# Performance work log

Measured on AMD Instinct MI355X. Metric: run time of the kernel, lower is better.

Reference implementation:

```python
import jax, jax.numpy as jnp
import numpy as np

B, N, IN_C, HID, K1, K2, OUT_C = 128, 512, 128, 32, 100, 10, 10
E_PER = 8192  # edges per graph (avg degree 16)
EPS = 1e-15


def _lin(key, fan_in, fan_out):
    return jax.random.normal(key, (fan_in, fan_out), jnp.float32) / np.sqrt(fan_in)


def setup_inputs() -> dict:
    key = jax.random.key(0)
    ks = jax.random.split(key, 20)
    total = B * N
    x = jax.random.normal(ks[0], (total, IN_C), jnp.float32)
    # per-graph random edges, offset into the global node index space
    src_l = jax.random.randint(ks[1], (B, E_PER), 0, N)
    dst_l = jax.random.randint(ks[2], (B, E_PER), 0, N)
    off = (jnp.arange(B, dtype=jnp.int32) * N)[:, None]
    edge_index = jnp.stack([(src_l + off).reshape(-1), (dst_l + off).reshape(-1)]).astype(jnp.int32)
    batch = (jnp.arange(total, dtype=jnp.int32) // N).astype(jnp.int32)
    return {
        "x": x,
        "edge_index": edge_index,
        "batch": batch,
        "conv1_W": _lin(ks[3], IN_C, HID), "conv1_b": jnp.zeros((HID,), jnp.float32),
        "pool1_W": _lin(ks[4], HID, K1), "pool1_b": jnp.zeros((K1,), jnp.float32),
        "conv2_rel_W": _lin(ks[5], HID, HID), "conv2_rel_b": jnp.zeros((HID,), jnp.float32),
        "conv2_root_W": _lin(ks[6], HID, HID),
        "pool2_W": _lin(ks[7], HID, K2), "pool2_b": jnp.zeros((K2,), jnp.float32),
        "conv3_rel_W": _lin(ks[8], HID, HID), "conv3_rel_b": jnp.zeros((HID,), jnp.float32),
        "conv3_root_W": _lin(ks[9], HID, HID),
        "lin1_W": _lin(ks[10], HID, HID), "lin1_b": jnp.zeros((HID,), jnp.float32),
        "lin2_W": _lin(ks[11], HID, OUT_C), "lin2_b": jnp.zeros((OUT_C,), jnp.float32),
    }


def gcn_conv(x, edge_index, W, b):
    # GCNConv with add_self_loops=True, symmetric normalization
    total = x.shape[0]
    loops = jnp.arange(total, dtype=edge_index.dtype)
    src = jnp.concatenate([edge_index[0], loops])
    dst = jnp.concatenate([edge_index[1], loops])
    w = jnp.ones(src.shape[0], x.dtype)
    deg = jax.ops.segment_sum(w, dst, num_segments=total)
    dis = jnp.where(deg > 0, jax.lax.rsqrt(deg), 0.0)
    norm = dis[src] * dis[dst]
    xw = x @ W
    out = jax.ops.segment_sum(norm[:, None] * xw[src], dst, num_segments=total)
    return out + b


def dense_mincut_pool(x, adj, s, mask=None):
    # x:[b,n,f] adj:[b,n,n] s:[b,n,k]
    s = jax.nn.softmax(s, axis=-1)
    if mask is not None:
        m = mask[..., None].astype(x.dtype)
        x = x * m
        s = s * m
    out = jnp.einsum('bnk,bnf->bkf', s, x)
    out_adj = jnp.einsum('bnk,bnm,bml->bkl', s, adj, s)
    mincut_num = jnp.trace(out_adj, axis1=-2, axis2=-1)
    d_flat = adj.sum(-1)  # [b,n]
    mincut_den = jnp.einsum('bnk,bn,bnk->b', s, d_flat, s)  # trace(s^T D s)
    mincut_loss = jnp.mean(-(mincut_num / mincut_den))
    k = s.shape[-1]
    ss = jnp.einsum('bnk,bnl->bkl', s, s)
    ss_norm = jnp.linalg.norm(ss, axis=(-1, -2), keepdims=True)
    i_s = jnp.eye(k, dtype=x.dtype) / jnp.sqrt(jnp.asarray(k, x.dtype))  # I_k / ||I_k||_F
    ortho_loss = jnp.mean(jnp.linalg.norm(ss / ss_norm - i_s, axis=(-1, -2)))
    # zero diagonal then symmetric degree-normalize
    out_adj = out_adj * (1.0 - jnp.eye(k, dtype=x.dtype))
    d = jnp.sqrt(out_adj.sum(-1))[..., None] + EPS
    out_adj = out_adj / d / jnp.swapaxes(d, -1, -2)
    return out, out_adj, mincut_loss, ortho_loss


def dense_graph_conv(x, adj, rel_W, rel_b, root_W):
    # DenseGraphConv(aggr='add'): lin_rel(adj @ x) + lin_root(x)
    return (adj @ x) @ rel_W + rel_b + x @ root_W


def reference(x, edge_index, batch, conv1_W, conv1_b, pool1_W, pool1_b,
              conv2_rel_W, conv2_rel_b, conv2_root_W, pool2_W, pool2_b,
              conv3_rel_W, conv3_rel_b, conv3_root_W, lin1_W, lin1_b, lin2_W, lin2_b):
    h = jax.nn.relu(gcn_conv(x, edge_index, conv1_W, conv1_b))
    # to_dense_batch: sorted batch with N nodes per graph -> reshape; mask all-true
    xd = h.reshape(B, N, HID)
    mask = jnp.ones((B, N), bool)
    # to_dense_adj
    b_idx = edge_index[0] // N
    s_l = edge_index[0] % N
    d_l = edge_index[1] % N
    adj = jnp.zeros((B, N, N), x.dtype).at[b_idx, s_l, d_l].add(1.0)
    s = xd @ pool1_W + pool1_b
    xd, adj, mc1, o1 = dense_mincut_pool(xd, adj, s, mask)
    xd = jax.nn.relu(dense_graph_conv(xd, adj, conv2_rel_W, conv2_rel_b, conv2_root_W))
    s = xd @ pool2_W + pool2_b
    xd, adj, mc2, o2 = dense_mincut_pool(xd, adj, s)
    xd = dense_graph_conv(xd, adj, conv3_rel_W, conv3_rel_b, conv3_root_W)
    g = xd.mean(axis=1)  # [B, HID]
    g = jax.nn.relu(g @ lin1_W + lin1_b)
    g = g @ lin2_W + lin2_b
    return jax.nn.log_softmax(g, axis=-1), mc1 + mc2 + o1 + o2
```

## Files before the change

### kernel.cpp

```cpp
#include <hip/hip_runtime.h>
#include <hip/hip_bf16.h>

#define TB   128
#define NN   512
#define INC  128
#define HH   32
#define KP1  100
#define KP2  10
#define OC   10
#define EPER 8192
#define NT   (TB*NN)
#define ET   (TB*EPER)
#define ZTR  264
#define ZTS  40
#define XTS  136

typedef unsigned int  u32;
typedef unsigned short u16;
typedef __attribute__((ext_vector_type(8))) short bf16x8;
typedef __attribute__((ext_vector_type(16))) float f32x16;

__device__ __forceinline__ u32 bfr(float f) {
    u32 b = __float_as_uint(f);
    return (b + 0x7fffu + ((b >> 16) & 1u)) >> 16;
}
__device__ __forceinline__ u32 pk2(float a, float b) { return bfr(a) | (bfr(b) << 16); }
__device__ __forceinline__ float blo(u32 u) { return __uint_as_float(u << 16); }
__device__ __forceinline__ float bhi(u32 u) { return __uint_as_float(u & 0xffff0000u); }

__global__ void k_init(float* __restrict__ aux) {
    int i = blockIdx.x * 256 + threadIdx.x;
    if (i < 1024) aux[i] = 0.0f;
}

__global__ __launch_bounds__(1024) void k_sort(const int* __restrict__ ei,
                                               int* __restrict__ cnt_src, int* __restrict__ cnt_dst,
                                               int* __restrict__ off_src, int* __restrict__ off_dst,
                                               u16* __restrict__ srt_dst, u16* __restrict__ srt_src,
                                               float* __restrict__ dis) {
    __shared__ int hs[NN], hd[NN], ps[NN], pd[NN];
    __shared__ __align__(16) u16 sdl[EPER], ssl[EPER];
    int g = blockIdx.x, tid = threadIdx.x, goff = g * NN;
    if (tid < NN) { hs[tid] = 0; hd[tid] = 0; }
    __syncthreads();
    const int* es = ei + (size_t)g * EPER;
    const int* ed = ei + ET + (size_t)g * EPER;
    for (int e = tid; e < EPER; e += 1024) {
        atomicAdd(&hs[es[e] - goff], 1);
        atomicAdd(&hd[ed[e] - goff], 1);
    }
    __syncthreads();
    int vs = 0, vd = 0;
    if (tid < NN) { vs = hs[tid]; vd = hd[tid]; ps[tid] = vs; pd[tid] = vd; }
    __syncthreads();
    for (int off = 1; off < NN; off <<= 1) {
        int xa = 0, xb = 0;
        if (tid < NN) {
            xa = ps[tid]; xb = pd[tid];
            if (tid >= off) { xa += ps[tid - off]; xb += pd[tid - off]; }
        }
        __syncthreads();
        if (tid < NN) { ps[tid] = xa; pd[tid] = xb; }
        __syncthreads();
    }
    int eso = 0, edo = 0;
    if (tid < NN) {
        eso = ps[tid] - vs; edo = pd[tid] - vd;
        cnt_src[goff + tid] = vs;  cnt_dst[goff + tid] = vd;
        off_src[goff + tid] = g * EPER + eso;
        off_dst[goff + tid] = g * EPER + edo;
        dis[goff + tid] = rsqrtf(1.0f + (float)vd);
    }
    __syncthreads();
    if (tid < NN) { ps[tid] = eso; pd[tid] = edo; }
    __syncthreads();
    for (int e = tid; e < EPER; e += 1024) {
        int s = es[e] - goff, d = ed[e] - goff;
        int p = atomicAdd(&ps[s], 1); sdl[p] = (u16)d;
        int q = atomicAdd(&pd[d], 1); ssl[q] = (u16)s;
    }
    __syncthreads();
    u32* wd = (u32*)(srt_dst + (size_t)g * EPER);
    u32* ws = (u32*)(srt_src + (size_t)g * EPER);
    const u32* rd = (const u32*)sdl;
    const u32* rs = (const u32*)ssl;
    for (int i = tid; i < EPER / 2; i += 1024) { wd[i] = rd[i]; ws[i] = rs[i]; }
}

__global__ __launch_bounds__(256) void k_xw2(const float* __restrict__ x, const float* __restrict__ W,
                                             u16* __restrict__ xwb) {
    __shared__ u16 sX[128 * XTS];
    __shared__ u16 sW[32 * XTS];
    int tid = threadIdx.x;
    int nbase = blockIdx.x * 128;
    for (int i = tid; i < INC * HH; i += 256) {
        int k = i >> 5, n = i & 31;
        sW[n * XTS + k] = (u16)bfr(W[i]);
    }
    for (int i = tid; i < 128 * 32; i += 256) {
        int r = i >> 5, q = i & 31;
        float4 v = ((const float4*)(x + (size_t)(nbase + r) * INC))[q];
        u32* dst = (u32*)&sX[r * XTS + q * 4];
        dst[0] = pk2(v.x, v.y);
        dst[1] = pk2(v.z, v.w);
    }
    __syncthreads();
    int wave = tid >> 6, lane = tid & 63;
    int lc = lane & 31, half = lane >> 5;
    f32x16 acc;
#pragma unroll
    for (int r = 0; r < 16; r++) acc[r] = 0.f;
#pragma unroll
    for (int kc = 0; kc < 8; kc++) {
        bf16x8 af  = *(const bf16x8*)&sX[(wave * 32 + lc) * XTS + kc * 16 + half * 8];
        bf16x8 bfv = *(const bf16x8*)&sW[lc * XTS + kc * 16 + half * 8];
        acc = __builtin_amdgcn_mfma_f32_32x32x16_bf16(af, bfv, acc, 0, 0, 0);
    }
#pragma unroll
    for (int r = 0; r < 16; r++) {
        int m = (r & 3) + 8 * (r >> 2) + 4 * half;
        int rowg = nbase + wave * 32 + m;
        xwb[(size_t)rowg * HH + lc] = (u16)bfr(acc[r]);
    }
}

__global__ __launch_bounds__(256) void k_gcng(const u16* __restrict__ ssrc, const int* __restrict__ od,
                                              const int* __restrict__ cd, const u32* __restrict__ xwb32,
                                              const float* __restrict__ dis, const float* __restrict__ bias,
                                              u32* __restrict__ hb32) {
    int tid = threadIdx.x;
    int b = blockIdx.x;
    int r8 = b & 7, j = b >> 3;
    int g = r8 + 8 * (j & 15);
    int chunk = j >> 4;
    int n = g * NN + chunk * 16 + (tid >> 4), cp = tid & 15;
    int goff = g * NN;
    int base = od[n], cnt = cd[n];
    float dn = dis[n];
    u32 us = xwb32[(size_t)n * 16 + cp];
    float a0 = dn * blo(us), a1 = dn * bhi(us);
    int i = 0;
    for (; i + 4 <= cnt; i += 4) {
        int s0 = goff + ssrc[base + i],     s1v = goff + ssrc[base + i + 1];
        int s2 = goff + ssrc[base + i + 2], s3  = goff + ssrc[base + i + 3];
        float d0 = dis[s0], d1 = dis[s1v], d2 = dis[s2], d3 = dis[s3];
        u32 u0 = xwb32[(size_t)s0 * 16 + cp];
        u32 u1 = xwb32[(size_t)s1v * 16 + cp];
        u32 u2 = xwb32[(size_t)s2 * 16 + cp];
        u32 u3 = xwb32[(size_t)s3 * 16 + cp];
        a0 += d0 * blo(u0) + d1 * blo(u1) + d2 * blo(u2) + d3 * blo(u3);
        a1 += d0 * bhi(u0) + d1 * bhi(u1) + d2 * bhi(u2) + d3 * bhi(u3);
    }
    for (; i < cnt; i++) {
        int s0 = goff + ssrc[base + i]; float d0 = dis[s0];
        u32 u0 = xwb32[(size_t)s0 * 16 + cp];
        a0 += d0 * blo(u0); a1 += d0 * bhi(u0);
    }
    float v0 = fmaxf(dn * a0 + bias[2 * cp], 0.f);
    float v1 = fmaxf(dn * a1 + bias[2 * cp + 1], 0.f);
    hb32[(size_t)n * 16 + cp] = pk2(v0, v1);
}

__global__ __launch_bounds__(256) void k_s1m(const u32* __restrict__ hb32, const float* __restrict__ W,
                                             const float* __restrict__ bias, const int* __restrict__ csrc,
                                             u16* __restrict__ s1b, float* __restrict__ den1) {
    __shared__ u16 sH[128 * ZTS];
    __shared__ u16 sW[128 * ZTS];
    int tid = threadIdx.x;
    int nbase = blockIdx.x * 128;
    for (int i = tid; i < HH * KP1; i += 256) {
        int k = i / KP1, n = i - k * KP1;
        sW[n * ZTS + k] = (u16)bfr(W[i]);
    }
    for (int i = tid; i < 28 * 16; i += 256) {
        int n = 100 + (i >> 4), q = i & 15;
        ((u32*)sW)[n * (ZTS / 2) + q] = 0;
    }
    for (int i = tid; i < 128 * 16; i += 256) {
        int r = i >> 4, q = i & 15;
        ((u32*)sH)[r * (ZTS / 2) + q] = hb32[(size_t)(nbase + r) * 16 + q];
    }
    __syncthreads();
    int wave = tid >> 6, lane = tid & 63;
    int lc = lane & 31, half = lane >> 5;
    f32x16 acc[4];
#pragma unroll
    for (int t = 0; t < 4; t++)
#pragma unroll
        for (int r = 0; r < 16; r++) acc[t][r] = 0.f;
#pragma unroll
    for (int kc = 0; kc < 2; kc++) {
        bf16x8 af = *(const bf16x8*)&sH[(wave * 32 + lc) * ZTS + kc * 16 + half * 8];
#pragma unroll
        for (int t = 0; t < 4; t++) {
            bf16x8 bfv = *(const bf16x8*)&sW[(t * 32 + lc) * ZTS + kc * 16 + half * 8];
            acc[t] = __builtin_amdgcn_mfma_f32_32x32x16_bf16(af, bfv, acc[t], 0, 0, 0);
        }
    }
    float s[16], q[16];
#pragma unroll
    for (int r = 0; r < 16; r++) { s[r] = 0.f; q[r] = 0.f; }
#pragma unroll
    for (int t = 0; t < 4; t++) {
        int ch = t * 32 + lc;
        bool valid = ch < KP1;
        float bv = valid ? bias[ch] : 0.f;
#pragma unroll
        for (int r = 0; r < 16; r++) {
            float ev = valid ? __expf(acc[t][r] + bv) : 0.f;
            acc[t][r] = ev; s[r] += ev; q[r] = fmaf(ev, ev, q[r]);
        }
    }
#pragma unroll
    for (int off = 16; off >= 1; off >>= 1) {
#pragma unroll
        for (int r = 0; r < 16; r++) { s[r] += __shfl_xor(s[r], off); q[r] += __shfl_xor(q[r], off); }
    }
    float inv[16];
#pragma unroll
    for (int r = 0; r < 16; r++) inv[r] = 1.f / s[r];
#pragma unroll
    for (int t = 0; t < 4; t++) {
        int ch = t * 32 + lc;
        if (ch < KP1) {
#pragma unroll
            for (int r = 0; r < 16; r++) {
                int lr = (r & 3) + 8 * (r >> 2) + 4 * half;
                int rowg = nbase + wave * 32 + lr;
                s1b[(size_t)rowg * KP1 + ch] = (u16)bfr(acc[t][r] * inv[r]);
            }
        }
    }
    float contrib = 0.f;
    if (lc == 0) {
#pragma unroll
        for (int r = 0; r < 16; r++) {
            int lr = (r & 3) + 8 * (r >> 2) + 4 * half;
            int rowg = nbase + wave * 32 + lr;
            contrib += (float)csrc[rowg] * q[r] * inv[r] * inv[r];
        }
    }
    contrib += __shfl_xor(contrib, 32);
    if (lane == 0) atomicAdd(&den1[nbase >> 9], contrib);
}

__global__ __launch_bounds__(256) void k_t1g(const u16* __restrict__ sdst, const int* __restrict__ osr,
                                             const int* __restrict__ csr, const u32* __restrict__ s1b32,
                                             u32* __restrict__ t1b32) {
    int tid = threadIdx.x;
    int b = blockIdx.x;
    int r8 = b & 7, j = b >> 3;
    int g = r8 + 8 * (j & 15);
    int chunk = j >> 4;
    int n = g * NN + chunk * 4 + (tid >> 6), lane = tid & 63;
    if (lane >= 50) return;
    int goff = g * NN;
    int base = osr[n], cnt = csr[n];
    float a0 = 0.f, a1 = 0.f;
    int i = 0;
    for (; i + 4 <= cnt; i += 4) {
        int d0 = goff + sdst[base + i],     d1 = goff + sdst[base + i + 1];
        int d2 = goff + sdst[base + i + 2], d3 = goff + sdst[base + i + 3];
        u32 u0 = s1b32[(size_t)d0 * 50 + lane];
        u32 u1 = s1b32[(size_t)d1 * 50 + lane];
        u32 u2 = s1b32[(size_t)d2 * 50 + lane];
        u32 u3 = s1b32[(size_t)d3 * 50 + lane];
        a0 += (blo(u0) + blo(u1)) + (blo(u2) + blo(u3));
        a1 += (bhi(u0) + bhi(u1)) + (bhi(u2) + bhi(u3));
    }
    for (; i < cnt; i++) {
        int d0 = goff + sdst[base + i];
        u32 u0 = s1b32[(size_t)d0 * 50 + lane];
        a0 += blo(u0); a1 += bhi(u0);
    }
    t1b32[(size_t)n * 50 + lane] = pk2(a0, a1);
}

__device__ __forceinline__ void ld_cp(const u32* __restrict__ sp, int rstr,
                                      u32& w0, u32& w1, u32& w2, u32& w3) {
    w0 = sp[0]; w1 = sp[rstr]; w2 = sp[2 * rstr]; w3 = sp[3 * rstr];
}
__device__ __forceinline__ void st_cp(u16* __restrict__ zb, int doff,
                                      u32 w0, u32 w1, u32 w2, u32 w3) {
    u32 lo01 = (w0 & 0xffffu) | (w1 << 16);
    u32 lo23 = (w2 & 0xffffu) | (w3 << 16);
    u32 hi01 = (w0 >> 16) | (w1 & 0xffff0000u);
    u32 hi23 = (w2 >> 16) | (w3 & 0xffff0000u);
    *(uint2*)&zb[doff]       = make_uint2(lo01, lo23);
    *(uint2*)&zb[doff + ZTS] = make_uint2(hi01, hi23);
}

#define GRAM_MFMA(zb)                                                                              \
    {                                                                                              \
        _Pragma("unroll")                                                                          \
        for (int mf = 0; mf < 2; mf++) {                                                           \
            bf16x8 af  = *(const bf16x8*)&(zb)[(132 + mt * 32 + lc) * ZTS + mf * 16 + half * 8];   \
            bf16x8 bv0 = *(const bf16x8*)&(zb)[((ct * 2    ) * 32 + lc) * ZTS + mf * 16 + half * 8]; \
            bf16x8 bv1 = *(const bf16x8*)&(zb)[((ct * 2 + 1) * 32 + lc) * ZTS + mf * 16 + half * 8]; \
            acc0 = __builtin_amdgcn_mfma_f32_32x32x16_bf16(af, bv0, acc0, 0, 0, 0);                \
            acc1 = __builtin_amdgcn_mfma_f32_32x32x16_bf16(af, bv1, acc1, 0, 0, 0);                \
        }                                                                                          \
    }

__global__ __launch_bounds__(1024, 1) void k_gram(const u32* __restrict__ s1b32, const u32* __restrict__ t1b32,
                                                  const u32* __restrict__ hb32,
                                                  float* __restrict__ A1n, float* __restrict__ P1,
                                                  float* __restrict__ aux) {
    __shared__ __align__(16) u16 sZ[2][ZTR * ZTS];
    __shared__ float sC[KP1 * 232];
    __shared__ float sRow[KP1], sd[KP1];
    __shared__ float sScal[3];
    int g = blockIdx.x;
    int nbase = g * NN;
    int tid = threadIdx.x;
    int wave = tid >> 6, lane = tid & 63;
    int mt = wave & 3;
    int ct = wave >> 2;
    int lc = lane & 31, half = lane >> 5;

    f32x16 acc0, acc1;
#pragma unroll
    for (int r = 0; r < 16; r++) { acc0[r] = 0.f; acc1[r] = 0.f; }

    int cp = (tid & 7) + ((tid >> 6) << 3);
    int rq = (tid >> 3) & 7;
    bool act = cp < 116;
    const u32* sp;
    int rstr;
    if (cp < 50)      { sp = t1b32 + cp;        rstr = 50; }
    else if (cp < 66) { sp = hb32 + (cp - 50);  rstr = 16; }
    else              { sp = s1b32 + (cp - 66); rstr = 50; }
    sp += (size_t)(nbase + rq * 4) * rstr;
    int step = rstr * 32;
    int doff = (2 * cp) * ZTS + rq * 4;

    if (tid < KP1) sRow[tid] = 0.f;
    if (tid < 3) sScal[tid] = 0.f;
    for (int i = tid; i < 32 * ZTS; i += 1024) {
        int r = 232 + i / ZTS, c = i % ZTS;
        sZ[0][r * ZTS + c] = 0; sZ[1][r * ZTS + c] = 0;
    }
    u32 a0, a1, a2, a3, b0 = 0, b1 = 0, b2 = 0, b3 = 0;
    if (act) {
        ld_cp(sp, rstr, a0, a1, a2, a3);
        st_cp(sZ[0], doff, a0, a1, a2, a3);
        sp += step;
        ld_cp(sp, rstr, b0, b1, b2, b3);
        sp += step;
    }
    __syncthreads();

    for (int nt = 0; nt < 16; nt += 2) {
        GRAM_MFMA(sZ[0]);
        if (act) {
            st_cp(sZ[1], doff, b0, b1, b2, b3);
            if (nt + 2 < 16) { ld_cp(sp, rstr, a0, a1, a2, a3); sp += step; }
        }
        __syncthreads();
        GRAM_MFMA(sZ[1]);
        if (act && nt + 2 < 16) {
            st_cp(sZ[0], doff, a0, a1, a2, a3);
            if (nt + 3 < 16) { ld_cp(sp, rstr, b0, b1, b2, b3); sp += step; }
        }
        __syncthreads();
    }
    {
        int l0 = (ct * 2) * 32 + lc;
        if (l0 < 232) {
#pragma unroll
            for (int r = 0; r < 16; r++) {
                int k = mt * 32 + (r & 3) + 8 * (r >> 2) + 4 * half;
                if (k < KP1) sC[k * 232 + l0] = acc0[r];
            }
        }
        int l1 = (ct * 2 + 1) * 32 + lc;
        if (l1 < 232) {
#pragma unroll
            for (int r = 0; r < 16; r++) {
                int k = mt * 32 + (r & 3) + 8 * (r >> 2) + 4 * half;
                if (k < KP1) sC[k * 232 + l1] = acc1[r];
            }
        }
    }
    __syncthreads();
    float ssq = 0.f, trss = 0.f, troa = 0.f;
    for (int idx = tid; idx < KP1 * 58; idx += 1024) {
        int k = idx / 58, q = idx - k * 58;
        float4 s = *(const float4*)&sC[k * 232 + q * 4];
        int c = q * 4;
        if (c < 100) {
            float rs = (s.x + s.y) + (s.z + s.w);
            if (k >= c && k < c + 4) { float d = ((const float*)&s)[k - c]; troa += d; rs -= d; }
            atomicAdd(&sRow[k], rs);
        } else if (c < 132) {
            *(float4*)&P1[((size_t)g * KP1 + k) * HH + (c - 100)] = s;
        } else {
            ssq += s.x * s.x + s.y * s.y + s.z * s.z + s.w * s.w;
            int l0 = c - 132;
            if (k >= l0 && k < l0 + 4) trss += ((const float*)&s)[k - l0];
        }
    }
#pragma unroll
    for (int off = 32; off >= 1; off >>= 1) {
        ssq  += __shfl_xor(ssq, off);
        trss += __shfl_xor(trss, off);
        troa += __shfl_xor(troa, off);
    }
    if ((tid & 63) == 0) {
        atomicAdd(&sScal[0], troa);
        atomicAdd(&sScal[1], trss);
        atomicAdd(&sScal[2], ssq);
    }
    __syncthreads();
    if (tid == 0) {
        float o1 = sqrtf(fmaxf(2.f - 2.f * sScal[1] / (sqrtf(sScal[2]) * 10.f), 0.f));
        aux[128 + g] = -(sScal[0] / aux[g]) + o1;
    }
    if (tid < KP1) sd[tid] = sqrtf(sRow[tid]) + 1e-15f;
    __syncthreads();
    for (int i = tid; i < KP1 * KP1; i += 1024) {
        int k = i / KP1, l = i - k * KP1;
        A1n[(size_t)g * (KP1 * KP1) + i] = (k == l) ? 0.f : sC[k * 232 + l] / (sd[k] * sd[l]);
    }
}

__global__ __launch_bounds__(512) void k_s2a(const float* __restrict__ A1n, const float* __restrict__ P1,
                                             const float* __restrict__ relW, const float* __restrict__ relB,
                                             const float* __restrict__ rootW,
                                             const float* __restrict__ p2W, const float* __restrict__ p2B,
                                             float* __restrict__ P2, float* __restrict__ A2n,
                                             float* __restrict__ aux) {
    __shared__ float sA[KP1 * KP1];
    __shared__ float sX[KP1 * HH];
    __shared__ float sY[KP1 * HH];
    __shared__ float sS2[KP1 * KP2];
    __shared__ float sT2[KP1 * KP2];
    __shared__ float sA2[100], sB2[100], sdd[10], red[100];
    int g = blockIdx.x, tid = threadIdx.x;
    const float* Ag = A1n + (size_t)g * (KP1 * KP1);
    for (int i = tid; i < KP1 * KP1 / 4; i += 512)
        ((float4*)sA)[i] = ((const float4*)Ag)[i];
    for (int i = tid; i < KP1 * HH; i += 512) sX[i] = P1[(size_t)g * (KP1 * HH) + i];
    __syncthreads();

    int n = tid >> 2, cq = tid & 3;
    if (tid < 400) {
        float yv[8];
#pragma unroll
        for (int j = 0; j < 8; j++) yv[j] = 0.f;
        for (int mq = 0; mq < 25; mq++) {
            float4 a4 = *(const float4*)&sA[n * KP1 + mq * 4];
            const float* xb = &sX[(mq * 4) * HH + cq * 8];
            float aa[4] = {a4.x, a4.y, a4.z, a4.w};
#pragma unroll
            for (int mm = 0; mm < 4; mm++) {
                const float* xr = xb + mm * HH;
#pragma unroll
                for (int j = 0; j < 8; j++) yv[j] = fmaf(aa[mm], xr[j], yv[j]);
            }
        }
#pragma unroll
        for (int j = 0; j < 8; j++) sY[n * HH + cq * 8 + j] = yv[j];
    }
    __syncthreads();
    float x2v[8];
    if (tid < 400) {
#pragma unroll
        for (int j = 0; j < 8; j++) x2v[j] = relB[cq * 8 + j];
        for (int j = 0; j < 32; j++) {
            float yj = sY[n * HH + j];
            float xj = sX[n * HH + j];
            float4 r0 = *(const float4*)&relW[j * 32 + cq * 8];
            float4 r1v = *(const float4*)&relW[j * 32 + cq * 8 + 4];
            float4 q0 = *(const float4*)&rootW[j * 32 + cq * 8];
            float4 q1 = *(const float4*)&rootW[j * 32 + cq * 8 + 4];
            x2v[0] += yj * r0.x + xj * q0.x;  x2v[1] += yj * r0.y + xj * q0.y;
            x2v[2] += yj * r0.z + xj * q0.z;  x2v[3] += yj * r0.w + xj * q0.w;
            x2v[4] += yj * r1v.x + xj * q1.x; x2v[5] += yj * r1v.y + xj * q1.y;
            x2v[6] += yj * r1v.z + xj * q1.z; x2v[7] += yj * r1v.w + xj * q1.w;
        }
    }
    __syncthreads();
    if (tid < 400) {
#pragma unroll
        for (int j = 0; j < 8; j++) sX[n * HH + cq * 8 + j] = fmaxf(x2v[j], 0.f);
    }
    __syncthreads();
    if (tid < KP1) {
        float lg[10];
#pragma unroll
        for (int j = 0; j < 10; j++) lg[j] = p2B[j];
        for (int c = 0; c < 32; c++) {
            float xv = sX[tid * HH + c];
#pragma unroll
            for (int j = 0; j < 10; j++) lg[j] = fmaf(xv, p2W[c * 10 + j], lg[j]);
        }
        float mx = lg[0];
#pragma unroll
        for (int j = 1; j < 10; j++) mx = fmaxf(mx, lg[j]);
        float se = 0.f;
#pragma unroll
        for (int j = 0; j < 10; j++) { lg[j] = __expf(lg[j] - mx); se += lg[j]; }
        float inv = 1.f / se, sq = 0.f;
#pragma unroll
        for (int j = 0; j < 10; j++) { float sv = lg[j] * inv; sS2[tid * 10 + j] = sv; sq += sv * sv; }
        float d2 = 0.f;
        for (int mq = 0; mq < 25; mq++) {
            float4 a4 = *(const float4*)&sA[tid * KP1 + mq * 4];
            d2 += a4.x + a4.y + a4.z + a4.w;
        }
        red[tid] = d2 * sq;
    }
    __syncthreads();
    for (int p = tid; p < KP1 * KP2; p += 512) {
        int n2 = p / 10, jj = p % 10;
        float a = 0.f;
        for (int m = 0; m < KP1; m++) a = fmaf(sA[n2 * KP1 + m], sS2[m * 10 + jj], a);
        sT2[p] = a;
    }
    if (tid < KP2 * HH) {
        int k = tid >> 5, cc = tid & 31;
        float a = 0.f;
        for (int n2 = 0; n2 < KP1; n2++) a = fmaf(sS2[n2 * 10 + k], sX[n2 * HH + cc], a);
        P2[(size_t)g * (KP2 * HH) + tid] = a;
    }
    __syncthreads();
    if (tid < 100) {
        int k = tid / 10, l = tid % 10;
        float oa = 0.f, ss = 0.f;
        for (int n2 = 0; n2 < KP1; n2++) {
            float sk = sS2[n2 * 10 + k];
            oa = fmaf(sk, sT2[n2 * 10 + l], oa);
            ss = fmaf(sk, sS2[n2 * 10 + l], ss);
        }
        sA2[tid] = oa; sB2[tid] = ss;
    }
    __syncthreads();
    if (tid == 0) {
        float den2 = 0.f;
        for (int i = 0; i < 100; i++) den2 += red[i];
        float troa = 0.f, trss = 0.f, ssq = 0.f;
        for (int k = 0; k < 10; k++) { troa += sA2[k * 10 + k]; trss += sB2[k * 10 + k]; }
        for (int i = 0; i < 100; i++) ssq += sB2[i] * sB2[i];
        float o2 = sqrtf(fmaxf(2.f - 2.f * trss / (sqrtf(ssq) * 3.16227766f), 0.f));
        aux[256 + g] = -(troa / den2) + o2;
    }
    if (tid < 10) {
        float rs = 0.f;
        for (int l = 0; l < 10; l++) if (l != tid) rs += sA2[tid * 10 + l];
        sdd[tid] = sqrtf(rs) + 1e-15f;
    }
    __syncthreads();
    if (tid < 100) {
        int k = tid / 10, l = tid % 10;
        A2n[(size_t)g * 100 + tid] = (k == l) ? 0.f : sA2[tid] / (sdd[k] * sdd[l]);
    }
}

__global__ __launch_bounds__(64) void k_s2b(const float* __restrict__ P2, const float* __restrict__ A2n,
                                            const float* __restrict__ relW3, const float* __restrict__ relb3,
                                            const float* __restrict__ rootW3,
                                            const float* __restrict__ l1W, const float* __restrict__ l1b,
                                            const float* __restrict__ l2W, const float* __restrict__ l2b,
                                            float* __restrict__ out) {
    __shared__ float sP[KP2 * HH], sA2[100], sY3[KP2 * HH], sG[32], sG1[32], sL[10], sLse;
    int g = blockIdx.x, tid = threadIdx.x;
    for (int i = tid; i < KP2 * HH; i += 64) sP[i] = P2[(size_t)g * (KP2 * HH) + i];
    for (int i = tid; i < 100; i += 64) sA2[i] = A2n[(size_t)g * 100 + i];
    if (tid < 32) sG[tid] = 0.f;
    __syncthreads();
    for (int p = tid; p < KP2 * HH; p += 64) {
        int k = p >> 5, cc = p & 31;
        float a = 0.f;
#pragma unroll
        for (int m = 0; m < 10; m++) a = fmaf(sA2[k * 10 + m], sP[m * HH + cc], a);
        sY3[p] = a;
    }
    __syncthreads();
    for (int p = tid; p < KP2 * HH; p += 64) {
        int k = p >> 5, cc = p & 31;
        float v = relb3[cc];
        for (int j = 0; j < 32; j++)
            v += sY3[k * HH + j] * relW3[j * 32 + cc] + sP[k * HH + j] * rootW3[j * 32 + cc];
        atomicAdd(&sG[cc], v * 0.1f);
    }
    __syncthreads();
    if (tid < 32) {
        float v = l1b[tid];
        for (int j = 0; j < 32; j++) v = fmaf(sG[j], l1W[j * 32 + tid], v);
        sG1[tid] = fmaxf(v, 0.f);
    }
    __syncthreads();
    if (tid < 10) {
        float v = l2b[tid];
        for (int j = 0; j < 32; j++) v = fmaf(sG1[j], l2W[j * 10 + tid], v);
        sL[tid] = v;
    }
    __syncthreads();
    if (tid == 0) {
        float mx = sL[0];
        for (int j = 1; j < 10; j++) mx = fmaxf(mx, sL[j]);
        float se = 0.f;
        for (int j = 0; j < 10; j++) se += expf(sL[j] - mx);
        sLse = mx + logf(se);
    }
    __syncthreads();
    if (tid < 10) out[(size_t)g * 10 + tid] = sL[tid] - sLse;
}

__global__ void k_loss(const float* __restrict__ aux, float* __restrict__ out) {
    __shared__ float red[128];
    int tid = threadIdx.x;
    red[tid] = aux[128 + tid] + aux[256 + tid];
    __syncthreads();
#pragma unroll
    for (int s = 64; s > 0; s >>= 1) { if (tid < s) red[tid] += red[tid + s]; __syncthreads(); }
    if (tid == 0) out[1280] = red[0] * (1.f / 128.f);
}

extern "C" void kernel_launch(void* const* d_in, const int* in_sizes, int n_in,
                              void* d_out, int out_size, void* d_ws, size_t ws_size,
                              hipStream_t stream) {
    const float* x    = (const float*)d_in[0];
    const int*   ei   = (const int*)d_in[1];
    const float* c1W  = (const float*)d_in[3];
    const float* c1b  = (const float*)d_in[4];
    const float* p1W  = (const float*)d_in[5];
    const float* p1b  = (const float*)d_in[6];
    const float* relW2  = (const float*)d_in[7];
    const float* relb2  = (const float*)d_in[8];
    const float* rootW2 = (const float*)d_in[9];
    const float* p2W  = (const float*)d_in[10];
    const float* p2b  = (const float*)d_in[11];
    const float* relW3  = (const float*)d_in[12];
    const float* relb3  = (const float*)d_in[13];
    const float* rootW3 = (const float*)d_in[14];
    const float* l1W  = (const float*)d_in[15];
    const float* l1b  = (const float*)d_in[16];
    const float* l2W  = (const float*)d_in[17];
    const float* l2b  = (const float*)d_in[18];
    float* out = (float*)d_out;

    int*  cnt_src = (int*)d_ws;
    int*  cnt_dst = cnt_src + NT;
    int*  off_src = cnt_dst + NT;
    int*  off_dst = off_src + NT;
    u16*  srt_dst = (u16*)(off_dst + NT);
    u16*  srt_src = srt_dst + ET;
    float* dis = (float*)(srt_src + ET);
    u32*  xwb  = (u32*)(dis + NT);
    u32*  hb   = xwb + (size_t)NT * 16;
    u32*  s1b  = hb + (size_t)NT * 16;
    u32*  t1b  = s1b + (size_t)NT * 50;
    float* A1n  = (float*)(t1b + (size_t)NT * 50);
    float* P1   = A1n + (size_t)TB * KP1 * KP1;
    float* P2   = P1 + (size_t)TB * KP1 * HH;
    float* A2n  = P2 + (size_t)TB * KP2 * HH;
    float* aux  = A2n + (size_t)TB * 100;

    k_init<<<4, 256, 0, stream>>>(aux);
    k_sort<<<TB, 1024, 0, stream>>>(ei, cnt_src, cnt_dst, off_src, off_dst, srt_dst, srt_src, dis);
    k_xw2<<<NT / 128, 256, 0, stream>>>(x, c1W, (u16*)xwb);
    k_gcng<<<NT / 16, 256, 0, stream>>>(srt_src, off_dst, cnt_dst, xwb, dis, c1b, hb);
    k_s1m<<<NT / 128, 256, 0, stream>>>(hb, p1W, p1b, cnt_src, (u16*)s1b, aux );
    k_t1g<<<NT / 4, 256, 0, stream>>>(srt_dst, off_src, cnt_src, s1b, t1b);
    k_gram<<<TB, 1024, 0, stream>>>(s1b, t1b, hb, A1n, P1, aux);
    k_s2a<<<TB, 512, 0, stream>>>(A1n, P1, relW2, relb2, rootW2, p2W, p2b, P2, A2n, aux);
    k_s2b<<<TB, 64, 0, stream>>>(P2, A2n, relW3, relb3, rootW3, l1W, l1b, l2W, l2b, out);
    k_loss<<<1, 128, 0, stream>>>(aux, out);
}
```

Before: 256.9 us.

## Fuse pooling tail kernels, fold aux init into sort, retile gram MFMA

Merges the second pooling stage and the final readout kernel into one kernel. P2 and the normalized A2 now stay in shared memory instead of round-tripping through global memory. The separate aux-zeroing kernel is removed, and each k_sort block now zeroes aux[g] itself, which is only correct if aux needs just 128 zeroed entries. The gram kernel is retiled so each wave computes a 2x2 block of 32x32 MFMA tiles over half the K range, reusing A and B fragments across more MFMAs. The two K halves are then summed in shared memory, at the cost of an extra barrier and a read-modify-write of the accumulators.

```diff
diff --git a/kernel.cpp b/kernel.cpp
--- a/kernel.cpp
+++ b/kernel.cpp
@@ -28,19 +28,15 @@
 __device__ __forceinline__ float blo(u32 u) { return __uint_as_float(u << 16); }
 __device__ __forceinline__ float bhi(u32 u) { return __uint_as_float(u & 0xffff0000u); }
 
-__global__ void k_init(float* __restrict__ aux) {
-    int i = blockIdx.x * 256 + threadIdx.x;
-    if (i < 1024) aux[i] = 0.0f;
-}
-
 __global__ __launch_bounds__(1024) void k_sort(const int* __restrict__ ei,
                                                int* __restrict__ cnt_src, int* __restrict__ cnt_dst,
                                                int* __restrict__ off_src, int* __restrict__ off_dst,
                                                u16* __restrict__ srt_dst, u16* __restrict__ srt_src,
-                                               float* __restrict__ dis) {
+                                               float* __restrict__ dis, float* __restrict__ aux) {
     __shared__ int hs[NN], hd[NN], ps[NN], pd[NN];
     __shared__ __align__(16) u16 sdl[EPER], ssl[EPER];
     int g = blockIdx.x, tid = threadIdx.x, goff = g * NN;
+    if (tid == 0) aux[g] = 0.f;
     if (tid < NN) { hs[tid] = 0; hd[tid] = 0; }
     __syncthreads();
     const int* es = ei + (size_t)g * EPER;
@@ -290,16 +286,31 @@
     *(uint2*)&zb[doff + ZTS] = make_uint2(hi01, hi23);
 }
 
-#define GRAM_MFMA(zb)                                                                              \
-    {                                                                                              \
-        _Pragma("unroll")                                                                          \
-        for (int mf = 0; mf < 2; mf++) {                                                           \
-            bf16x8 af  = *(const bf16x8*)&(zb)[(132 + mt * 32 + lc) * ZTS + mf * 16 + half * 8];   \
-            bf16x8 bv0 = *(const bf16x8*)&(zb)[((ct * 2    ) * 32 + lc) * ZTS + mf * 16 + half * 8]; \
-            bf16x8 bv1 = *(const bf16x8*)&(zb)[((ct * 2 + 1) * 32 + lc) * ZTS + mf * 16 + half * 8]; \
-            acc0 = __builtin_amdgcn_mfma_f32_32x32x16_bf16(af, bv0, acc0, 0, 0, 0);                \
-            acc1 = __builtin_amdgcn_mfma_f32_32x32x16_bf16(af, bv1, acc1, 0, 0, 0);                \
-        }                                                                                          \
+#define GRAM_MFMA(zb)                                                                               \
+    {                                                                                               \
+        bf16x8 af0 = *(const bf16x8*)&(zb)[(132 + (2*mtb    )*32 + lc)*ZTS + mfh*16 + half*8];      \
+        bf16x8 af1 = *(const bf16x8*)&(zb)[(132 + (2*mtb + 1)*32 + lc)*ZTS + mfh*16 + half*8];      \
+        bf16x8 bv0 = *(const bf16x8*)&(zb)[((2*ctb    )*32 + lc)*ZTS + mfh*16 + half*8];            \
+        bf16x8 bv1 = *(const bf16x8*)&(zb)[((2*ctb + 1)*32 + lc)*ZTS + mfh*16 + half*8];            \
+        acc00 = __builtin_amdgcn_mfma_f32_32x32x16_bf16(af0, bv0, acc00, 0, 0, 0);                  \
+        acc01 = __builtin_amdgcn_mfma_f32_32x32x16_bf16(af0, bv1, acc01, 0, 0, 0);                  \
+        acc10 = __builtin_amdgcn_mfma_f32_32x32x16_bf16(af1, bv0, acc10, 0, 0, 0);                  \
+        acc11 = __builtin_amdgcn_mfma_f32_32x32x16_bf16(af1, bv1, acc11, 0, 0, 0);                  \
+    }
+
+#define DUMP_TILE(AV, MT, CT, ADD)                                                                  \
+    {                                                                                               \
+        int l = (CT) * 32 + lc;                                                                     \
+        if (l < 232) {                                                                              \
+            _Pragma("unroll")                                                                       \
+            for (int r = 0; r < 16; r++) {                                                          \
+                int k = (MT) * 32 + (r & 3) + 8 * (r >> 2) + 4 * half;                              \
+                if (k < KP1) {                                                                      \
+                    if (ADD) sC[k * 232 + l] += AV[r];                                              \
+                    else     sC[k * 232 + l] = AV[r];                                               \
+                }                                                                                   \
+            }                                                                                       \
+        }                                                                                           \
     }
 
 __global__ __launch_bounds__(1024, 1) void k_gram(const u32* __restrict__ s1b32, const u32* __restrict__ t1b32,
@@ -314,13 +325,14 @@
     int nbase = g * NN;
     int tid = threadIdx.x;
     int wave = tid >> 6, lane = tid & 63;
-    int mt = wave & 3;
-    int ct = wave >> 2;
+    int mfh = wave & 1;
+    int mtb = (wave >> 1) & 1;
+    int ctb = wave >> 2;
     int lc = lane & 31, half = lane >> 5;
 
-    f32x16 acc0, acc1;
-#pragma unroll
-    for (int r = 0; r < 16; r++) { acc0[r] = 0.f; acc1[r] = 0.f; }
+    f32x16 acc00, acc01, acc10, acc11;
+#pragma unroll
+    for (int r = 0; r < 16; r++) { acc00[r] = 0.f; acc01[r] = 0.f; acc10[r] = 0.f; acc11[r] = 0.f; }
 
     int cp = (tid & 7) + ((tid >> 6) << 3);
     int rq = (tid >> 3) & 7;
@@ -364,23 +376,18 @@
         }
         __syncthreads();
     }
-    {
-        int l0 = (ct * 2) * 32 + lc;
-        if (l0 < 232) {
-#pragma unroll
-            for (int r = 0; r < 16; r++) {
-                int k = mt * 32 + (r & 3) + 8 * (r >> 2) + 4 * half;
-                if (k < KP1) sC[k * 232 + l0] = acc0[r];
-            }
-        }
-        int l1 = (ct * 2 + 1) * 32 + lc;
-        if (l1 < 232) {
-#pragma unroll
-            for (int r = 0; r < 16; r++) {
-                int k = mt * 32 + (r & 3) + 8 * (r >> 2) + 4 * half;
-                if (k < KP1) sC[k * 232 + l1] = acc1[r];
-            }
-        }
+    if (mfh == 0) {
+        DUMP_TILE(acc00, 2 * mtb,     2 * ctb,     0)
+        DUMP_TILE(acc01, 2 * mtb,     2 * ctb + 1, 0)
+        DUMP_TILE(acc10, 2 * mtb + 1, 2 * ctb,     0)
+        DUMP_TILE(acc11, 2 * mtb + 1, 2 * ctb + 1, 0)
+    }
+    __syncthreads();
+    if (mfh == 1) {
+        DUMP_TILE(acc00, 2 * mtb,     2 * ctb,     1)
+        DUMP_TILE(acc01, 2 * mtb,     2 * ctb + 1, 1)
+        DUMP_TILE(acc10, 2 * mtb + 1, 2 * ctb,     1)
+        DUMP_TILE(acc11, 2 * mtb + 1, 2 * ctb + 1, 1)
     }
     __syncthreads();
     float ssq = 0.f, trss = 0.f, troa = 0.f;
@@ -424,23 +431,28 @@
     }
 }
 
-__global__ __launch_bounds__(512) void k_s2a(const float* __restrict__ A1n, const float* __restrict__ P1,
-                                             const float* __restrict__ relW, const float* __restrict__ relB,
-                                             const float* __restrict__ rootW,
-                                             const float* __restrict__ p2W, const float* __restrict__ p2B,
-                                             float* __restrict__ P2, float* __restrict__ A2n,
-                                             float* __restrict__ aux) {
+__global__ __launch_bounds__(512) void k_s2(const float* __restrict__ A1n, const float* __restrict__ P1,
+                                            const float* __restrict__ relW, const float* __restrict__ relB,
+                                            const float* __restrict__ rootW,
+                                            const float* __restrict__ p2W, const float* __restrict__ p2B,
+                                            const float* __restrict__ relW3, const float* __restrict__ relb3,
+                                            const float* __restrict__ rootW3,
+                                            const float* __restrict__ l1W, const float* __restrict__ l1b,
+                                            const float* __restrict__ l2W, const float* __restrict__ l2b,
+                                            float* __restrict__ out, float* __restrict__ aux) {
     __shared__ float sA[KP1 * KP1];
     __shared__ float sX[KP1 * HH];
     __shared__ float sY[KP1 * HH];
     __shared__ float sS2[KP1 * KP2];
     __shared__ float sT2[KP1 * KP2];
     __shared__ float sA2[100], sB2[100], sdd[10], red[100];
+    __shared__ float sP2[KP2 * HH], sAn[100], sY3[KP2 * HH], sG[32], sG1[32], sL[10], sLse;
     int g = blockIdx.x, tid = threadIdx.x;
     const float* Ag = A1n + (size_t)g * (KP1 * KP1);
     for (int i = tid; i < KP1 * KP1 / 4; i += 512)
         ((float4*)sA)[i] = ((const float4*)Ag)[i];
     for (int i = tid; i < KP1 * HH; i += 512) sX[i] = P1[(size_t)g * (KP1 * HH) + i];
+    if (tid < 32) sG[tid] = 0.f;
     __syncthreads();
 
     int n = tid >> 2, cq = tid & 3;
@@ -522,7 +534,7 @@
         int k = tid >> 5, cc = tid & 31;
         float a = 0.f;
         for (int n2 = 0; n2 < KP1; n2++) a = fmaf(sS2[n2 * 10 + k], sX[n2 * HH + cc], a);
-        P2[(size_t)g * (KP2 * HH) + tid] = a;
+        sP2[tid] = a;
     }
     __syncthreads();
     if (tid < 100) {
@@ -553,35 +565,22 @@
     __syncthreads();
     if (tid < 100) {
         int k = tid / 10, l = tid % 10;
-        A2n[(size_t)g * 100 + tid] = (k == l) ? 0.f : sA2[tid] / (sdd[k] * sdd[l]);
-    }
-}
-
-__global__ __launch_bounds__(64) void k_s2b(const float* __restrict__ P2, const float* __restrict__ A2n,
-                                            const float* __restrict__ relW3, const float* __restrict__ relb3,
-                                            const float* __restrict__ rootW3,
-                                            const float* __restrict__ l1W, const float* __restrict__ l1b,
-                                            const float* __restrict__ l2W, const float* __restrict__ l2b,
-                                            float* __restrict__ out) {
-    __shared__ float sP[KP2 * HH], sA2[100], sY3[KP2 * HH], sG[32], sG1[32], sL[10], sLse;
-    int g = blockIdx.x, tid = threadIdx.x;
-    for (int i = tid; i < KP2 * HH; i += 64) sP[i] = P2[(size_t)g * (KP2 * HH) + i];
-    for (int i = tid; i < 100; i += 64) sA2[i] = A2n[(size_t)g * 100 + i];
-    if (tid < 32) sG[tid] = 0.f;
-    __syncthreads();
-    for (int p = tid; p < KP2 * HH; p += 64) {
-        int k = p >> 5, cc = p & 31;
+        sAn[tid] = (k == l) ? 0.f : sA2[tid] / (sdd[k] * sdd[l]);
+    }
+    __syncthreads();
+    if (tid < KP2 * HH) {
+        int k = tid >> 5, cc = tid & 31;
         float a = 0.f;
 #pragma unroll
-        for (int m = 0; m < 10; m++) a = fmaf(sA2[k * 10 + m], sP[m * HH + cc], a);
-        sY3[p] = a;
-    }
-    __syncthreads();
-    for (int p = tid; p < KP2 * HH; p += 64) {
-        int k = p >> 5, cc = p & 31;
+        for (int m = 0; m < 10; m++) a = fmaf(sAn[k * 10 + m], sP2[m * HH + cc], a);
+        sY3[tid] = a;
+    }
+    __syncthreads();
+    if (tid < KP2 * HH) {
+        int k = tid >> 5, cc = tid & 31;
         float v = relb3[cc];
         for (int j = 0; j < 32; j++)
-            v += sY3[k * HH + j] * relW3[j * 32 + cc] + sP[k * HH + j] * rootW3[j * 32 + cc];
+            v += sY3[k * HH + j] * relW3[j * 32 + cc] + sP2[k * HH + j] * rootW3[j * 32 + cc];
         atomicAdd(&sG[cc], v * 0.1f);
     }
     __syncthreads();
@@ -654,18 +653,15 @@
     u32*  t1b  = s1b + (size_t)NT * 50;
     float* A1n  = (float*)(t1b + (size_t)NT * 50);
     float* P1   = A1n + (size_t)TB * KP1 * KP1;
-    float* P2   = P1 + (size_t)TB * KP1 * HH;
-    float* A2n  = P2 + (size_t)TB * KP2 * HH;
-    float* aux  = A2n + (size_t)TB * 100;
-
-    k_init<<<4, 256, 0, stream>>>(aux);
-    k_sort<<<TB, 1024, 0, stream>>>(ei, cnt_src, cnt_dst, off_src, off_dst, srt_dst, srt_src, dis);
+    float* aux  = P1 + (size_t)TB * KP1 * HH;
+
+    k_sort<<<TB, 1024, 0, stream>>>(ei, cnt_src, cnt_dst, off_src, off_dst, srt_dst, srt_src, dis, aux);
     k_xw2<<<NT / 128, 256, 0, stream>>>(x, c1W, (u16*)xwb);
     k_gcng<<<NT / 16, 256, 0, stream>>>(srt_src, off_dst, cnt_dst, xwb, dis, c1b, hb);
     k_s1m<<<NT / 128, 256, 0, stream>>>(hb, p1W, p1b, cnt_src, (u16*)s1b, aux );
     k_t1g<<<NT / 4, 256, 0, stream>>>(srt_dst, off_src, cnt_src, s1b, t1b);
     k_gram<<<TB, 1024, 0, stream>>>(s1b, t1b, hb, A1n, P1, aux);
-    k_s2a<<<TB, 512, 0, stream>>>(A1n, P1, relW2, relb2, rootW2, p2W, p2b, P2, A2n, aux);
-    k_s2b<<<TB, 64, 0, stream>>>(P2, A2n, relW3, relb3, rootW3, l1W, l1b, l2W, l2b, out);
+    k_s2<<<TB, 512, 0, stream>>>(A1n, P1, relW2, relb2, rootW2, p2W, p2b,
+                                 relW3, relb3, rootW3, l1W, l1b, l2W, l2b, out, aux);
     k_loss<<<1, 128, 0, stream>>>(aux, out);
 }
```

New measurement: 250.1 us. 1.03x faster.
